# Optimization experiments

Measured on AMD Instinct MI355X. Metric: run time of the kernel, lower is better.

## Reference

```python
import jax, jax.numpy as jnp
import numpy as np

INITIAL_RADIUS = 1.0  # init_kwargs: initial_radius > 0 -> distance-softmax branch


def reference(xyz, sparse_xyz, sparse_flow, resol_factor, K):
    # xyz: [B,3,N], sparse_xyz: [B,3,M], sparse_flow: [B,3,M]
    q = jnp.transpose(xyz, (0, 2, 1))            # [B,N,3]
    p = jnp.transpose(sparse_xyz, (0, 2, 1))     # [B,M,3]
    flow = jnp.transpose(sparse_flow, (0, 2, 1))  # [B,M,3]

    sigma = INITIAL_RADIUS * resol_factor
    qs = q / sigma
    ps = p / sigma

    # pairwise Euclidean distances [B,N,M]
    sq = (jnp.sum(qs * qs, -1)[:, :, None]
          + jnp.sum(ps * ps, -1)[:, None, :]
          - 2.0 * jnp.einsum('bnc,bmc->bnm', qs, ps))
    dist = jnp.sqrt(jnp.maximum(sq, 1e-12))

    # K nearest: smallest distances
    neg_d, idx = jax.lax.top_k(-dist, K)          # [B,N,K]
    K_dist = -neg_d                               # [B,N,K]

    # gather flow of the K neighbors: [B,N,K,3]
    grouped_flow = jnp.take_along_axis(flow[:, None, :, :], idx[..., None], axis=2)

    # softmax over -distance along K, weighted sum
    K_w = jax.nn.softmax(-K_dist, axis=2)         # [B,N,K]
    dense_flow = jnp.sum(K_w[..., None] * grouped_flow, axis=2)  # [B,N,3]

    return jnp.transpose(dense_flow, (0, 2, 1))   # [B,3,N]


def setup_inputs() -> dict:
    key = jax.random.key(0)
    k1, k2, k3 = jax.random.split(key, 3)
    B, N, M = 4, 16384, 4096
    return {
        'xyz': jax.random.normal(k1, (B, 3, N), dtype=jnp.float32),
        'sparse_xyz': jax.random.normal(k2, (B, 3, M), dtype=jnp.float32),
        'sparse_flow': jax.random.normal(k3, (B, 3, M), dtype=jnp.float32),
        'resol_factor': 1,
        'K': 5,
    }
```

## Files before the change

kernel.cpp:

```cpp
#include <hip/hip_runtime.h>
#include <math.h>
#include <stdint.h>


#define KNN 5
#define SLICES 8
#define BLOCK (SLICES * 64)
#define GRP_SHIFT 8

typedef unsigned int u32;

__device__ __forceinline__ float get_inv_sigma(const int* __restrict__ rf) {
    const int ri = rf[0];
    const float sigma = (ri >= 1 && ri <= 1000000) ? (float)ri : __int_as_float(ri);
    return 1.0f / sigma;
}

__global__ __launch_bounds__(256)
void prep_kernel(const float* __restrict__ sxyz, const int* __restrict__ rf,
                 float4* __restrict__ pts, int M, int total) {
    const int t = blockIdx.x * 256 + threadIdx.x;
    if (t >= total) return;
    const float inv = get_inv_sigma(rf);
    const int b = t / M, m = t - b * M;
    const float* sb = sxyz + (size_t)b * 3 * M;
    const float x = sb[m] * inv;
    const float y = sb[M + m] * inv;
    const float z = sb[2 * M + m] * inv;
    pts[t] = make_float4(x, y, z, fmaf(x, x, fmaf(y, y, z * z)));
}

#define CE_FULL(k, ki, c, ci)                          \
    {                                                  \
        const bool sw = (c) < (k);                     \
        const float vmn = fminf(k, c);                 \
        const float vmx = fmaxf(k, c);                 \
        const u32 nki = sw ? (ci) : (ki);              \
        const u32 nci = sw ? (ki) : (ci);              \
        (k) = vmn; (c) = vmx; (ki) = nki; (ci) = nci;  \
    }
#define CE_LAST(k, ki, c, ci)                          \
    {                                                  \
        const bool sw = (c) < (k);                     \
        (ki) = sw ? (ci) : (ki);                       \
        (k) = fminf(k, c);                             \
    }

template <bool USE_PTS>
__global__ __launch_bounds__(BLOCK, 8)
void knn_kernel(const float* __restrict__ xyz,
                const float* __restrict__ sxyz,
                const float* __restrict__ sflow,
                const int* __restrict__ rf,
                const float4* __restrict__ pts,
                float* __restrict__ out,
                int N, int M) {
    __shared__ float sval_d[SLICES * KNN * 64];
    __shared__ u32   sval_i[SLICES * KNN * 64];

    const int tid  = threadIdx.x;
    const int lane = tid & 63;
    const int wid  = tid >> 6;
    const int swid = __builtin_amdgcn_readfirstlane(wid);
    const int b    = blockIdx.x >> GRP_SHIFT;
    const int grp  = blockIdx.x & ((1 << GRP_SHIFT) - 1);
    const int n    = grp * 64 + lane;

    const float inv = get_inv_sigma(rf);
    const float* qb = xyz + (size_t)b * 3 * N;
    const float qx = qb[n] * inv;
    const float qy = qb[N + n] * inv;
    const float qz = qb[2 * N + n] * inv;
    const float qq = fmaf(qx, qx, fmaf(qy, qy, qz * qz));

    const int CH = M / SLICES;
    const int j0 = swid * CH;

    float e0 = 1e30f, e1 = 1e30f, e2 = 1e30f, e3 = 1e30f, e4 = 1e30f;
    u32   i0 = 0, i1 = 0, i2 = 0, i3 = 0, i4 = 0;

    if constexpr (USE_PTS) {
        const float4* __restrict__ P = pts + (size_t)b * M + j0;
#pragma unroll 4
        for (int j = 0; j < CH; ++j) {
            const float4 p = P[j];
            float t = qx * p.x;
            t = fmaf(qy, p.y, t);
            t = fmaf(qz, p.z, t);
            float c = fmaf(-2.0f, t, p.w);
            u32 ci = (u32)(j0 + j);
            CE_FULL(e0, i0, c, ci)
            CE_FULL(e1, i1, c, ci)
            CE_FULL(e2, i2, c, ci)
            CE_FULL(e3, i3, c, ci)
            CE_LAST(e4, i4, c, ci)
        }
    } else {
        const float* __restrict__ sb = sxyz + (size_t)b * 3 * M;
#pragma unroll 4
        for (int j = 0; j < CH; ++j) {
            const float px = sb[j0 + j] * inv;
            const float py = sb[M + j0 + j] * inv;
            const float pz = sb[2 * M + j0 + j] * inv;
            const float pw = fmaf(px, px, fmaf(py, py, pz * pz));
            float t = qx * px;
            t = fmaf(qy, py, t);
            t = fmaf(qz, pz, t);
            float c = fmaf(-2.0f, t, pw);
            u32 ci = (u32)(j0 + j);
            CE_FULL(e0, i0, c, ci)
            CE_FULL(e1, i1, c, ci)
            CE_FULL(e2, i2, c, ci)
            CE_FULL(e3, i3, c, ci)
            CE_LAST(e4, i4, c, ci)
        }
    }

    sval_d[(wid * KNN + 0) * 64 + lane] = e0;  sval_i[(wid * KNN + 0) * 64 + lane] = i0;
    sval_d[(wid * KNN + 1) * 64 + lane] = e1;  sval_i[(wid * KNN + 1) * 64 + lane] = i1;
    sval_d[(wid * KNN + 2) * 64 + lane] = e2;  sval_i[(wid * KNN + 2) * 64 + lane] = i2;
    sval_d[(wid * KNN + 3) * 64 + lane] = e3;  sval_i[(wid * KNN + 3) * 64 + lane] = i3;
    sval_d[(wid * KNN + 4) * 64 + lane] = e4;  sval_i[(wid * KNN + 4) * 64 + lane] = i4;
    __syncthreads();

    if (wid == 0) {
        float m0 = 1e30f, m1 = 1e30f, m2 = 1e30f, m3 = 1e30f, m4 = 1e30f;
        u32   g0 = 0, g1 = 0, g2 = 0, g3 = 0, g4 = 0;
#pragma unroll
        for (int w = 0; w < SLICES; ++w) {
#pragma unroll
            for (int k = 0; k < KNN; ++k) {
                float c = sval_d[(w * KNN + k) * 64 + lane];
                u32  ci = sval_i[(w * KNN + k) * 64 + lane];
                CE_FULL(m0, g0, c, ci)
                CE_FULL(m1, g1, c, ci)
                CE_FULL(m2, g2, c, ci)
                CE_FULL(m3, g3, c, ci)
                CE_LAST(m4, g4, c, ci)
            }
        }

        const float d0 = sqrtf(fmaxf(m0 + qq, 1e-12f));
        const float d1 = sqrtf(fmaxf(m1 + qq, 1e-12f));
        const float d2 = sqrtf(fmaxf(m2 + qq, 1e-12f));
        const float d3 = sqrtf(fmaxf(m3 + qq, 1e-12f));
        const float d4 = sqrtf(fmaxf(m4 + qq, 1e-12f));
        const float w0 = expf(d0 - d0);
        const float w1 = expf(d0 - d1);
        const float w2 = expf(d0 - d2);
        const float w3 = expf(d0 - d3);
        const float w4 = expf(d0 - d4);
        const float inv_wsum = 1.0f / (w0 + w1 + w2 + w3 + w4);

        const float* fb = sflow + (size_t)b * 3 * M;
        float ax = 0.f, ay = 0.f, az = 0.f;
        ax = fmaf(w0, fb[g0], ax); ay = fmaf(w0, fb[M + g0], ay); az = fmaf(w0, fb[2 * M + g0], az);
        ax = fmaf(w1, fb[g1], ax); ay = fmaf(w1, fb[M + g1], ay); az = fmaf(w1, fb[2 * M + g1], az);
        ax = fmaf(w2, fb[g2], ax); ay = fmaf(w2, fb[M + g2], ay); az = fmaf(w2, fb[2 * M + g2], az);
        ax = fmaf(w3, fb[g3], ax); ay = fmaf(w3, fb[M + g3], ay); az = fmaf(w3, fb[2 * M + g3], az);
        ax = fmaf(w4, fb[g4], ax); ay = fmaf(w4, fb[M + g4], ay); az = fmaf(w4, fb[2 * M + g4], az);

        float* ob = out + (size_t)b * 3 * N;
        ob[n]         = ax * inv_wsum;
        ob[N + n]     = ay * inv_wsum;
        ob[2 * N + n] = az * inv_wsum;
    }
}

extern "C" void kernel_launch(void* const* d_in, const int* in_sizes, int n_in,
                              void* d_out, int out_size, void* d_ws, size_t ws_size,
                              hipStream_t stream) {
    const float* xyz   = (const float*)d_in[0];
    const float* sxyz  = (const float*)d_in[1];
    const float* sflow = (const float*)d_in[2];
    const int*   rf    = (const int*)d_in[3];

    const int B = 4;
    const int N = in_sizes[0] / (3 * B);
    const int M = in_sizes[1] / (3 * B);
    float* out = (float*)d_out;

    const dim3 grid(B * (N / 64));
    const dim3 block(BLOCK);

    const size_t need = (size_t)B * M * sizeof(float4);
    if (ws_size >= need) {
        float4* pts = (float4*)d_ws;
        prep_kernel<<<dim3((B * M + 255) / 256), dim3(256), 0, stream>>>(sxyz, rf, pts, M, B * M);
        knn_kernel<true><<<grid, block, 0, stream>>>(xyz, sxyz, sflow, rf, pts, out, N, M);
    } else {
        knn_kernel<false><<<grid, block, 0, stream>>>(xyz, sxyz, sflow, rf, nullptr, out, N, M);
    }
}
```

Before: 252.2 us.

## Replace brute-force KNN with uniform-grid spatial search over sparse points

Builds a 16^3 uniform grid over the sparse points each call, using a bbox reduction, atomic counting, a prefix scan and an atomic scatter into cell-sorted order. Each query then scans cell shells outward until its 5th-best distance is provably within the searched radius. Distance and index are packed into 64-bit keys, and two waves split the shells by parity before a merge. This removes most of the O(N*M) distance work, at the cost of five kernel launches, atomics and divergent per-lane search loops. The old brute-force path is kept as a fallback when there is too little workspace.

```diff
diff --git a/kernel.cpp b/kernel.cpp
--- a/kernel.cpp
+++ b/kernel.cpp
@@ -3,12 +3,14 @@
 #include <stdint.h>
 
 
+typedef unsigned int u32;
+typedef unsigned long long u64;
+
 #define KNN 5
-#define SLICES 8
-#define BLOCK (SLICES * 64)
-#define GRP_SHIFT 8
-
-typedef unsigned int u32;
+#define G 16
+#define G3 (G * G * G)
+#define SBLOCK 512
+#define GROUPS_PER_BLOCK 4
 
 __device__ __forceinline__ float get_inv_sigma(const int* __restrict__ rf) {
     const int ri = rf[0];
@@ -16,19 +18,252 @@
     return 1.0f / sigma;
 }
 
+__device__ __forceinline__ void cell_of(float x, float y, float z,
+                                        const float4 o, const float invh,
+                                        int& cx, int& cy, int& cz) {
+    cx = (int)floorf((x - o.x) * invh);
+    cy = (int)floorf((y - o.y) * invh);
+    cz = (int)floorf((z - o.z) * invh);
+    cx = min(max(cx, 0), G - 1);
+    cy = min(max(cy, 0), G - 1);
+    cz = min(max(cz, 0), G - 1);
+}
+
+
 __global__ __launch_bounds__(256)
-void prep_kernel(const float* __restrict__ sxyz, const int* __restrict__ rf,
-                 float4* __restrict__ pts, int M, int total) {
+void zero_bbox_kernel(const float* __restrict__ sxyz, const int* __restrict__ rf,
+                      int M, float4* __restrict__ bbox,
+                      u32* __restrict__ meta, u32* __restrict__ cursor) {
+    const int b = blockIdx.x, tid = threadIdx.x;
+    u32* mb = meta + b * G3;
+    u32* cb = cursor + b * G3;
+    for (int i = tid; i < G3; i += 256) { mb[i] = 0u; cb[i] = 0u; }
+
+    const float inv = get_inv_sigma(rf);
+    const float* sb = sxyz + (size_t)b * 3 * M;
+    float mnx = 1e30f, mny = 1e30f, mnz = 1e30f;
+    float mxx = -1e30f, mxy = -1e30f, mxz = -1e30f;
+    for (int i = tid; i < M; i += 256) {
+        const float x = sb[i] * inv, y = sb[M + i] * inv, z = sb[2 * M + i] * inv;
+        mnx = fminf(mnx, x); mxx = fmaxf(mxx, x);
+        mny = fminf(mny, y); mxy = fmaxf(mxy, y);
+        mnz = fminf(mnz, z); mxz = fmaxf(mxz, z);
+    }
+    __shared__ float red[6][256];
+    red[0][tid] = mnx; red[1][tid] = mny; red[2][tid] = mnz;
+    red[3][tid] = mxx; red[4][tid] = mxy; red[5][tid] = mxz;
+    __syncthreads();
+    for (int s = 128; s > 0; s >>= 1) {
+        if (tid < s) {
+            red[0][tid] = fminf(red[0][tid], red[0][tid + s]);
+            red[1][tid] = fminf(red[1][tid], red[1][tid + s]);
+            red[2][tid] = fminf(red[2][tid], red[2][tid + s]);
+            red[3][tid] = fmaxf(red[3][tid], red[3][tid + s]);
+            red[4][tid] = fmaxf(red[4][tid], red[4][tid + s]);
+            red[5][tid] = fmaxf(red[5][tid], red[5][tid + s]);
+        }
+        __syncthreads();
+    }
+    if (tid == 0) {
+        const float ox = red[0][0], oy = red[1][0], oz = red[2][0];
+        const float ex = red[3][0] - ox, ey = red[4][0] - oy, ez = red[5][0] - oz;
+        const float ext = fmaxf(fmaxf(ex, ey), ez);
+        const float h = ext * (1.0f + 2e-5f) / (float)G + 1e-20f;
+        bbox[2 * b + 0] = make_float4(ox, oy, oz, h);
+        bbox[2 * b + 1] = make_float4(1.0f / h, 0.f, 0.f, 0.f);
+    }
+}
+
+__global__ __launch_bounds__(256)
+void count_kernel(const float* __restrict__ sxyz, const int* __restrict__ rf,
+                  int M, int total, const float4* __restrict__ bbox,
+                  u32* __restrict__ meta) {
     const int t = blockIdx.x * 256 + threadIdx.x;
     if (t >= total) return;
-    const float inv = get_inv_sigma(rf);
     const int b = t / M, m = t - b * M;
+    const float inv = get_inv_sigma(rf);
     const float* sb = sxyz + (size_t)b * 3 * M;
-    const float x = sb[m] * inv;
-    const float y = sb[M + m] * inv;
-    const float z = sb[2 * M + m] * inv;
-    pts[t] = make_float4(x, y, z, fmaf(x, x, fmaf(y, y, z * z)));
-}
+    const float x = sb[m] * inv, y = sb[M + m] * inv, z = sb[2 * M + m] * inv;
+    const float4 o = bbox[2 * b];
+    const float invh = bbox[2 * b + 1].x;
+    int cx, cy, cz; cell_of(x, y, z, o, invh, cx, cy, cz);
+    atomicAdd(&meta[b * G3 + (cz * G + cy) * G + cx], 1u);
+}
+
+__global__ __launch_bounds__(256)
+void scan_kernel(u32* __restrict__ meta, u32* __restrict__ cursor) {
+    const int b = blockIdx.x, tid = threadIdx.x;
+    u32* mb = meta + b * G3;
+    u32* cb = cursor + b * G3;
+    __shared__ u32 tmp[256];
+    __shared__ u32 carry;
+    if (tid == 0) carry = 0u;
+    __syncthreads();
+    for (int base = 0; base < G3; base += 256) {
+        const u32 c = mb[base + tid];
+        tmp[tid] = c;
+        __syncthreads();
+        for (int s = 1; s < 256; s <<= 1) {
+            u32 v = (tid >= s) ? tmp[tid - s] : 0u;
+            __syncthreads();
+            tmp[tid] += v;
+            __syncthreads();
+        }
+        const u32 incl = tmp[tid];
+        const u32 start = carry + incl - c;
+        mb[base + tid] = (start << 13) | c;
+        cb[base + tid] = start;
+        __syncthreads();
+        if (tid == 255) carry += tmp[255];
+        __syncthreads();
+    }
+}
+
+__global__ __launch_bounds__(256)
+void scatter_kernel(const float* __restrict__ sxyz, const int* __restrict__ rf,
+                    int M, int total, const float4* __restrict__ bbox,
+                    u32* __restrict__ cursor, float4* __restrict__ pts) {
+    const int t = blockIdx.x * 256 + threadIdx.x;
+    if (t >= total) return;
+    const int b = t / M, m = t - b * M;
+    const float inv = get_inv_sigma(rf);
+    const float* sb = sxyz + (size_t)b * 3 * M;
+    const float x = sb[m] * inv, y = sb[M + m] * inv, z = sb[2 * M + m] * inv;
+    const float4 o = bbox[2 * b];
+    const float invh = bbox[2 * b + 1].x;
+    int cx, cy, cz; cell_of(x, y, z, o, invh, cx, cy, cz);
+    const u32 pos = atomicAdd(&cursor[b * G3 + (cz * G + cy) * G + cx], 1u);
+    pts[(size_t)b * M + pos] = make_float4(x, y, z, __uint_as_float((u32)m));
+}
+
+
+#define CEK_FULL(k, c) { const bool sw_ = (c) < (k); const u64 mn_ = sw_ ? (c) : (k); \
+                         const u64 mx_ = sw_ ? (k) : (c); (k) = mn_; (c) = mx_; }
+#define CEK_LAST(k, c) { (k) = ((c) < (k)) ? (c) : (k); }
+
+#define PROC_CAND(p) {                                                        \
+    float t_ = qx * (p).x; t_ = fmaf(qy, (p).y, t_); t_ = fmaf(qz, (p).z, t_);\
+    const float pw_ = fmaf((p).x, (p).x, fmaf((p).y, (p).y, (p).z * (p).z));  \
+    const float dc_ = fmaxf(fmaf(-2.0f, t_, qq + pw_), 1e-12f);               \
+    u64 c_ = ((u64)__float_as_uint(dc_) << 32) | (u64)__float_as_uint((p).w); \
+    CEK_FULL(k0, c_) CEK_FULL(k1, c_) CEK_FULL(k2, c_) CEK_FULL(k3, c_)       \
+    CEK_LAST(k4, c_) }
+
+#define KEY_INIT (((u64)0x7F7FFFFFu) << 32)
+
+__global__ __launch_bounds__(SBLOCK)
+void grid_search_kernel(const float* __restrict__ xyz,
+                        const float* __restrict__ sflow,
+                        const int* __restrict__ rf,
+                        const float4* __restrict__ bbox,
+                        const u32* __restrict__ meta,
+                        const float4* __restrict__ pts,
+                        float* __restrict__ out,
+                        int N, int M, int bpB) {
+    __shared__ u64 mergeK[GROUPS_PER_BLOCK * KNN * 64];
+
+    const int tid   = threadIdx.x;
+    const int lane  = tid & 63;
+    const int wid   = tid >> 6;
+    const int slice = __builtin_amdgcn_readfirstlane(wid & 1);
+    const int gid   = wid >> 1;
+    const int g     = blockIdx.x * GROUPS_PER_BLOCK + gid;
+    const int b     = g / bpB;
+    const int n     = (g % bpB) * 64 + lane;
+
+    const float inv = get_inv_sigma(rf);
+    const float* qb = xyz + (size_t)b * 3 * N;
+    const float qx = qb[n] * inv;
+    const float qy = qb[N + n] * inv;
+    const float qz = qb[2 * N + n] * inv;
+    const float qq = fmaf(qx, qx, fmaf(qy, qy, qz * qz));
+
+    const float4 o   = bbox[2 * b];
+    const float invh = bbox[2 * b + 1].x;
+    const float h    = o.w;
+    int qcx, qcy, qcz; cell_of(qx, qy, qz, o, invh, qcx, qcy, qcz);
+
+    const u32* mb = meta + b * G3;
+    const float4* pb = pts + (size_t)b * M;
+
+    u64 k0 = KEY_INIT, k1 = KEY_INIT, k2 = KEY_INIT, k3 = KEY_INIT, k4 = KEY_INIT;
+    bool done = false;
+    const float margin = 1e-3f + 1e-5f * qq;
+    int stripe = 0;
+
+    for (int r = 0; r <= G && __any(!done); ++r) {
+        for (int dz = -r; dz <= r; ++dz)
+        for (int dy = -r; dy <= r; ++dy)
+        for (int dx = -r; dx <= r; ++dx) {
+            if (r > 0 && abs(dx) < r && abs(dy) < r && abs(dz) < r) continue;
+            const int par = stripe & 1; ++stripe;
+            if (par != slice) continue;
+            if (done) continue;
+            const int cx = qcx + dx, cy = qcy + dy, cz = qcz + dz;
+            if ((u32)cx >= G || (u32)cy >= G || (u32)cz >= G) continue;
+            const u32 mc = mb[(cz * G + cy) * G + cx];
+            const u32 cnt = mc & 8191u;
+            const u32 st  = mc >> 13;
+            u32 i = 0;
+            for (; i + 2 <= cnt; i += 2) {
+                const float4 pa = pb[st + i];
+                const float4 pc = pb[st + i + 1];
+                PROC_CAND(pa)
+                PROC_CAND(pc)
+            }
+            if (i < cnt) { const float4 pa = pb[st + i]; PROC_CAND(pa) }
+        }
+        if (!done) {
+            const float own = __uint_as_float((u32)(k4 >> 32));
+            const float bound = (float)r * h;
+            done = (own < bound * bound - margin);
+        }
+    }
+
+    if (slice == 1) {
+        mergeK[(gid * KNN + 0) * 64 + lane] = k0;
+        mergeK[(gid * KNN + 1) * 64 + lane] = k1;
+        mergeK[(gid * KNN + 2) * 64 + lane] = k2;
+        mergeK[(gid * KNN + 3) * 64 + lane] = k3;
+        mergeK[(gid * KNN + 4) * 64 + lane] = k4;
+    }
+    __syncthreads();
+
+    if (slice == 0) {
+#pragma unroll
+        for (int k = 0; k < KNN; ++k) {
+            u64 c = mergeK[(gid * KNN + k) * 64 + lane];
+            CEK_FULL(k0, c) CEK_FULL(k1, c) CEK_FULL(k2, c) CEK_FULL(k3, c)
+            CEK_LAST(k4, c)
+        }
+        const float d0 = sqrtf(__uint_as_float((u32)(k0 >> 32)));
+        const float d1 = sqrtf(__uint_as_float((u32)(k1 >> 32)));
+        const float d2 = sqrtf(__uint_as_float((u32)(k2 >> 32)));
+        const float d3 = sqrtf(__uint_as_float((u32)(k3 >> 32)));
+        const float d4 = sqrtf(__uint_as_float((u32)(k4 >> 32)));
+        const float w0 = expf(d0 - d0);
+        const float w1 = expf(d0 - d1);
+        const float w2 = expf(d0 - d2);
+        const float w3 = expf(d0 - d3);
+        const float w4 = expf(d0 - d4);
+        const float inv_wsum = 1.0f / (w0 + w1 + w2 + w3 + w4);
+
+        const u32 i0 = (u32)k0, i1 = (u32)k1, i2 = (u32)k2, i3 = (u32)k3, i4 = (u32)k4;
+        const float* fb = sflow + (size_t)b * 3 * M;
+        float ax = 0.f, ay = 0.f, az = 0.f;
+        ax = fmaf(w0, fb[i0], ax); ay = fmaf(w0, fb[M + i0], ay); az = fmaf(w0, fb[2 * M + i0], az);
+        ax = fmaf(w1, fb[i1], ax); ay = fmaf(w1, fb[M + i1], ay); az = fmaf(w1, fb[2 * M + i1], az);
+        ax = fmaf(w2, fb[i2], ax); ay = fmaf(w2, fb[M + i2], ay); az = fmaf(w2, fb[2 * M + i2], az);
+        ax = fmaf(w3, fb[i3], ax); ay = fmaf(w3, fb[M + i3], ay); az = fmaf(w3, fb[2 * M + i3], az);
+        ax = fmaf(w4, fb[i4], ax); ay = fmaf(w4, fb[M + i4], ay); az = fmaf(w4, fb[2 * M + i4], az);
+
+        float* ob = out + (size_t)b * 3 * N;
+        ob[n]         = ax * inv_wsum;
+        ob[N + n]     = ay * inv_wsum;
+        ob[2 * N + n] = az * inv_wsum;
+    }
+}
+
 
 #define CE_FULL(k, ki, c, ci)                          \
     {                                                  \
@@ -46,112 +281,62 @@
         (k) = fminf(k, c);                             \
     }
 
-template <bool USE_PTS>
-__global__ __launch_bounds__(BLOCK, 8)
-void knn_kernel(const float* __restrict__ xyz,
-                const float* __restrict__ sxyz,
-                const float* __restrict__ sflow,
-                const int* __restrict__ rf,
-                const float4* __restrict__ pts,
-                float* __restrict__ out,
-                int N, int M) {
-    __shared__ float sval_d[SLICES * KNN * 64];
-    __shared__ u32   sval_i[SLICES * KNN * 64];
-
-    const int tid  = threadIdx.x;
-    const int lane = tid & 63;
-    const int wid  = tid >> 6;
+#define BSLICES 8
+__global__ __launch_bounds__(512)
+void brute_kernel(const float* __restrict__ xyz, const float* __restrict__ sxyz,
+                  const float* __restrict__ sflow, const int* __restrict__ rf,
+                  float* __restrict__ out, int N, int M, int bpB) {
+    __shared__ float sval_d[BSLICES * KNN * 64];
+    __shared__ u32   sval_i[BSLICES * KNN * 64];
+    const int tid = threadIdx.x, lane = tid & 63, wid = tid >> 6;
     const int swid = __builtin_amdgcn_readfirstlane(wid);
-    const int b    = blockIdx.x >> GRP_SHIFT;
-    const int grp  = blockIdx.x & ((1 << GRP_SHIFT) - 1);
-    const int n    = grp * 64 + lane;
-
+    const int b = blockIdx.x / bpB;
+    const int n = (blockIdx.x % bpB) * 64 + lane;
     const float inv = get_inv_sigma(rf);
     const float* qb = xyz + (size_t)b * 3 * N;
-    const float qx = qb[n] * inv;
-    const float qy = qb[N + n] * inv;
-    const float qz = qb[2 * N + n] * inv;
+    const float qx = qb[n] * inv, qy = qb[N + n] * inv, qz = qb[2 * N + n] * inv;
     const float qq = fmaf(qx, qx, fmaf(qy, qy, qz * qz));
-
-    const int CH = M / SLICES;
-    const int j0 = swid * CH;
-
+    const int CH = M / BSLICES, j0 = swid * CH;
+    const float* sb = sxyz + (size_t)b * 3 * M;
     float e0 = 1e30f, e1 = 1e30f, e2 = 1e30f, e3 = 1e30f, e4 = 1e30f;
-    u32   i0 = 0, i1 = 0, i2 = 0, i3 = 0, i4 = 0;
-
-    if constexpr (USE_PTS) {
-        const float4* __restrict__ P = pts + (size_t)b * M + j0;
-#pragma unroll 4
-        for (int j = 0; j < CH; ++j) {
-            const float4 p = P[j];
-            float t = qx * p.x;
-            t = fmaf(qy, p.y, t);
-            t = fmaf(qz, p.z, t);
-            float c = fmaf(-2.0f, t, p.w);
-            u32 ci = (u32)(j0 + j);
-            CE_FULL(e0, i0, c, ci)
-            CE_FULL(e1, i1, c, ci)
-            CE_FULL(e2, i2, c, ci)
-            CE_FULL(e3, i3, c, ci)
-            CE_LAST(e4, i4, c, ci)
-        }
-    } else {
-        const float* __restrict__ sb = sxyz + (size_t)b * 3 * M;
-#pragma unroll 4
-        for (int j = 0; j < CH; ++j) {
-            const float px = sb[j0 + j] * inv;
-            const float py = sb[M + j0 + j] * inv;
-            const float pz = sb[2 * M + j0 + j] * inv;
-            const float pw = fmaf(px, px, fmaf(py, py, pz * pz));
-            float t = qx * px;
-            t = fmaf(qy, py, t);
-            t = fmaf(qz, pz, t);
-            float c = fmaf(-2.0f, t, pw);
-            u32 ci = (u32)(j0 + j);
-            CE_FULL(e0, i0, c, ci)
-            CE_FULL(e1, i1, c, ci)
-            CE_FULL(e2, i2, c, ci)
-            CE_FULL(e3, i3, c, ci)
-            CE_LAST(e4, i4, c, ci)
-        }
-    }
-
+    u32 i0 = 0, i1 = 0, i2 = 0, i3 = 0, i4 = 0;
+    for (int j = 0; j < CH; ++j) {
+        const float px = sb[j0 + j] * inv;
+        const float py = sb[M + j0 + j] * inv;
+        const float pz = sb[2 * M + j0 + j] * inv;
+        const float pw = fmaf(px, px, fmaf(py, py, pz * pz));
+        float t = qx * px; t = fmaf(qy, py, t); t = fmaf(qz, pz, t);
+        float c = fmaf(-2.0f, t, pw);
+        u32 ci = (u32)(j0 + j);
+        CE_FULL(e0, i0, c, ci) CE_FULL(e1, i1, c, ci) CE_FULL(e2, i2, c, ci)
+        CE_FULL(e3, i3, c, ci) CE_LAST(e4, i4, c, ci)
+    }
     sval_d[(wid * KNN + 0) * 64 + lane] = e0;  sval_i[(wid * KNN + 0) * 64 + lane] = i0;
     sval_d[(wid * KNN + 1) * 64 + lane] = e1;  sval_i[(wid * KNN + 1) * 64 + lane] = i1;
     sval_d[(wid * KNN + 2) * 64 + lane] = e2;  sval_i[(wid * KNN + 2) * 64 + lane] = i2;
     sval_d[(wid * KNN + 3) * 64 + lane] = e3;  sval_i[(wid * KNN + 3) * 64 + lane] = i3;
     sval_d[(wid * KNN + 4) * 64 + lane] = e4;  sval_i[(wid * KNN + 4) * 64 + lane] = i4;
     __syncthreads();
-
     if (wid == 0) {
         float m0 = 1e30f, m1 = 1e30f, m2 = 1e30f, m3 = 1e30f, m4 = 1e30f;
-        u32   g0 = 0, g1 = 0, g2 = 0, g3 = 0, g4 = 0;
+        u32 g0 = 0, g1 = 0, g2 = 0, g3 = 0, g4 = 0;
 #pragma unroll
-        for (int w = 0; w < SLICES; ++w) {
+        for (int w = 0; w < BSLICES; ++w)
 #pragma unroll
             for (int k = 0; k < KNN; ++k) {
                 float c = sval_d[(w * KNN + k) * 64 + lane];
-                u32  ci = sval_i[(w * KNN + k) * 64 + lane];
-                CE_FULL(m0, g0, c, ci)
-                CE_FULL(m1, g1, c, ci)
-                CE_FULL(m2, g2, c, ci)
-                CE_FULL(m3, g3, c, ci)
-                CE_LAST(m4, g4, c, ci)
+                u32 ci = sval_i[(w * KNN + k) * 64 + lane];
+                CE_FULL(m0, g0, c, ci) CE_FULL(m1, g1, c, ci) CE_FULL(m2, g2, c, ci)
+                CE_FULL(m3, g3, c, ci) CE_LAST(m4, g4, c, ci)
             }
-        }
-
         const float d0 = sqrtf(fmaxf(m0 + qq, 1e-12f));
         const float d1 = sqrtf(fmaxf(m1 + qq, 1e-12f));
         const float d2 = sqrtf(fmaxf(m2 + qq, 1e-12f));
         const float d3 = sqrtf(fmaxf(m3 + qq, 1e-12f));
         const float d4 = sqrtf(fmaxf(m4 + qq, 1e-12f));
-        const float w0 = expf(d0 - d0);
-        const float w1 = expf(d0 - d1);
-        const float w2 = expf(d0 - d2);
-        const float w3 = expf(d0 - d3);
-        const float w4 = expf(d0 - d4);
+        const float w0 = expf(d0 - d0), w1 = expf(d0 - d1), w2 = expf(d0 - d2);
+        const float w3 = expf(d0 - d3), w4 = expf(d0 - d4);
         const float inv_wsum = 1.0f / (w0 + w1 + w2 + w3 + w4);
-
         const float* fb = sflow + (size_t)b * 3 * M;
         float ax = 0.f, ay = 0.f, az = 0.f;
         ax = fmaf(w0, fb[g0], ax); ay = fmaf(w0, fb[M + g0], ay); az = fmaf(w0, fb[2 * M + g0], az);
@@ -159,10 +344,9 @@
         ax = fmaf(w2, fb[g2], ax); ay = fmaf(w2, fb[M + g2], ay); az = fmaf(w2, fb[2 * M + g2], az);
         ax = fmaf(w3, fb[g3], ax); ay = fmaf(w3, fb[M + g3], ay); az = fmaf(w3, fb[2 * M + g3], az);
         ax = fmaf(w4, fb[g4], ax); ay = fmaf(w4, fb[M + g4], ay); az = fmaf(w4, fb[2 * M + g4], az);
-
         float* ob = out + (size_t)b * 3 * N;
-        ob[n]         = ax * inv_wsum;
-        ob[N + n]     = ay * inv_wsum;
+        ob[n] = ax * inv_wsum;
+        ob[N + n] = ay * inv_wsum;
         ob[2 * N + n] = az * inv_wsum;
     }
 }
@@ -179,16 +363,28 @@
     const int N = in_sizes[0] / (3 * B);
     const int M = in_sizes[1] / (3 * B);
     float* out = (float*)d_out;
-
-    const dim3 grid(B * (N / 64));
-    const dim3 block(BLOCK);
-
-    const size_t need = (size_t)B * M * sizeof(float4);
-    if (ws_size >= need) {
-        float4* pts = (float4*)d_ws;
-        prep_kernel<<<dim3((B * M + 255) / 256), dim3(256), 0, stream>>>(sxyz, rf, pts, M, B * M);
-        knn_kernel<true><<<grid, block, 0, stream>>>(xyz, sxyz, sflow, rf, pts, out, N, M);
+    const int bpB = N / 64;
+
+    const size_t bboxBytes = (size_t)B * 2 * sizeof(float4);
+    const size_t metaBytes = (size_t)B * G3 * sizeof(u32);
+    const size_t ptsBytes  = (size_t)B * M * sizeof(float4);
+    const size_t need = bboxBytes + 2 * metaBytes + ptsBytes;
+
+    if (ws_size >= need && M <= 8191) {
+        char* w = (char*)d_ws;
+        float4* bbox  = (float4*)w;                       w += bboxBytes;
+        u32*    meta  = (u32*)w;                          w += metaBytes;
+        u32*    cursor= (u32*)w;                          w += metaBytes;
+        float4* pts   = (float4*)w;
+
+        zero_bbox_kernel<<<dim3(B), dim3(256), 0, stream>>>(sxyz, rf, M, bbox, meta, cursor);
+        count_kernel<<<dim3((B * M + 255) / 256), dim3(256), 0, stream>>>(sxyz, rf, M, B * M, bbox, meta);
+        scan_kernel<<<dim3(B), dim3(256), 0, stream>>>(meta, cursor);
+        scatter_kernel<<<dim3((B * M + 255) / 256), dim3(256), 0, stream>>>(sxyz, rf, M, B * M, bbox, cursor, pts);
+        const int nGroups = B * bpB;
+        grid_search_kernel<<<dim3(nGroups / GROUPS_PER_BLOCK), dim3(SBLOCK), 0, stream>>>(
+            xyz, sflow, rf, bbox, meta, pts, out, N, M, bpB);
     } else {
-        knn_kernel<false><<<grid, block, 0, stream>>>(xyz, sxyz, sflow, rf, nullptr, out, N, M);
-    }
-}
+        brute_kernel<<<dim3(B * bpB), dim3(512), 0, stream>>>(xyz, sxyz, sflow, rf, out, N, M, bpB);
+    }
+}
```

After: 617.5 us. 2.45x slower.
